# Performance work log

Hardware: AMD Instinct MI355X
Metric: run time of the kernel (lower is better)

Reference implementation:

```python
import jax, jax.numpy as jnp
import numpy as np

# ---- CRF hyperparameters (init_kwargs) ----
NUM_CLASSES = 4
RADIUS = 10            # guided filter radius -> 21x21 kernel
EPS = 1e-4
THETA_GAMMA = 2.5
G_RADIUS = int(THETA_GAMMA * 4)  # gaussian layer radius = 10 -> 21x21 kernel
SPATIAL_COMPAT = 3.0
BILATERAL_COMPAT = 10.0
NUM_ITERATIONS = 5
RGB_W = np.array([0.2989, 0.5870, 0.1140], dtype=np.float32)  # tf rgb_to_grayscale


def _make_kernel(radius, theta):
    x, y = np.mgrid[-radius:radius + 1, -radius:radius + 1]
    k = np.exp(-(x ** 2 + y ** 2) / (2.0 * theta ** 2))
    k = k / k.sum()
    k[radius, radius] = 0.0  # zero out center (no self-message)
    return jnp.asarray(k, dtype=jnp.float32)

_GAUSS_K = _make_kernel(G_RADIUS, THETA_GAMMA)          # spatial gaussian kernel
_GUIDED_K = _make_kernel(RADIUS, RADIUS / 3.0)          # guided-filter gaussian kernel


def _depthwise(src, k2d, r):
    # src: [B,H,W,C], k2d: [kh,kw]; zero-padded depthwise conv (same as pad+VALID)
    c = src.shape[-1]
    kh, kw = k2d.shape
    k = jnp.broadcast_to(k2d[:, :, None, None], (kh, kw, 1, c))
    return jax.lax.conv_general_dilated(
        src, k, window_strides=(1, 1), padding=[(r, r), (r, r)],
        dimension_numbers=('NHWC', 'HWIO', 'NHWC'), feature_group_count=c)


def _gaussian(src):
    return _depthwise(src, _GAUSS_K, G_RADIUS)


def _guided(gray, p):
    # guided gaussian filter with single-channel guide `gray` [B,H,W,1]
    gf = lambda s: _depthwise(s, _GUIDED_K, RADIUS)
    mean_I = gf(gray)                       # [B,H,W,1]
    mean_p = gf(p)                          # [B,H,W,C]
    mean_Ip = gf(gray * p)
    cov_Ip = mean_Ip - mean_I * mean_p
    mean_II = gf(gray * gray)
    var_I = mean_II - mean_I * mean_I
    a = cov_Ip / (var_I + EPS)
    b = mean_p - a * mean_I
    return gf(a) * gray + gf(b)


def setup_inputs() -> dict:
    key = jax.random.key(0)
    k1, k2 = jax.random.split(key)
    unary = jax.random.normal(k1, (1, 512, 512, NUM_CLASSES), dtype=jnp.float32)
    image = jax.random.uniform(k2, (1, 512, 512, 3), dtype=jnp.float32)
    return {"unary": unary, "image": image}


def reference(unary, image):
    gray = (image @ jnp.asarray(RGB_W))[..., None]        # [B,H,W,1]
    ones = jnp.ones_like(unary)
    spatial_norm = _gaussian(ones)
    bilateral_norm = _guided(gray, ones)

    Q = jax.nn.softmax(-unary, axis=-1)
    for _ in range(NUM_ITERATIONS):
        spatial_out = _gaussian(Q) / spatial_norm
        bilateral_out = _guided(gray, Q) / bilateral_norm
        # spatial_weights = SPATIAL_COMPAT*I, bilateral_weights = BILATERAL_COMPAT*I,
        # compatibility = -I  => matmuls reduce to scalar scaling + negation
        message = SPATIAL_COMPAT * spatial_out + BILATERAL_COMPAT * bilateral_out
        pairwise = -message
        Q = jax.nn.softmax(-unary - pairwise, axis=-1)
    return Q
```

## Files before the change

kernel.cpp:

```cpp
#include <hip/hip_runtime.h>
#include <math.h>

#define W 512
#define H 512
#define NPIX (W*H)
#define RAD 10
#define KS 21
#define CRF_EPS 1e-4f

#define TX 32
#define TY 16
#define CIN (TX + 2*RAD)
#define RIN (TY + 2*RAD)
#define GX (W / TX)
#define GY (H / TY)
#define NBLK (GX*GY)

struct W21 { float w[KS]; };

__device__ __forceinline__ float4 f4(float x, float y, float z, float w_) {
    return make_float4(x, y, z, w_);
}
__device__ __forceinline__ float4 fma4(float s, float4 a, float4 acc) {
    acc.x = fmaf(s, a.x, acc.x); acc.y = fmaf(s, a.y, acc.y);
    acc.z = fmaf(s, a.z, acc.z); acc.w = fmaf(s, a.w, acc.w);
    return acc;
}
__device__ __forceinline__ int swz(int b, int N) {
    return (b & 7) * (N >> 3) + (b >> 3);
}


__global__ __launch_bounds__(512) void k_tables(W21 wg, W21 wu, float* Sg, float* Su) {
    int x = threadIdx.x;
    float sg = 0.f, su = 0.f;
    #pragma unroll
    for (int d = -RAD; d <= RAD; ++d) {
        int xx = x + d;
        if (xx >= 0 && xx < W) { sg += wg.w[d + RAD]; su += wu.w[d + RAD]; }
    }
    Sg[x] = sg; Su[x] = su;
}

__global__ __launch_bounds__(256) void k_init(const float* __restrict__ img,
        const float4* __restrict__ unary, float* __restrict__ gray,
        float4* __restrict__ Q) {
    int b = swz(blockIdx.x, NPIX / 256);
    int p = b * 256 + threadIdx.x;
    float r = img[3 * p], g = img[3 * p + 1], bch = img[3 * p + 2];
    gray[p] = 0.2989f * r + 0.5870f * g + 0.1140f * bch;
    float4 u = unary[p];
    float mn = fminf(fminf(u.x, u.y), fminf(u.z, u.w));
    float ex = expf(mn - u.x), ey = expf(mn - u.y), ez = expf(mn - u.z), ew = expf(mn - u.w);
    float inv = 1.f / (ex + ey + ez + ew);
    Q[p] = f4(ex * inv, ey * inv, ez * inv, ew * inv);
}

__global__ __launch_bounds__(256) void k_s1(const float* __restrict__ gray,
        const float* __restrict__ Su, float* __restrict__ mean_I,
        float* __restrict__ inv_var, float2* __restrict__ a1b1,
        W21 wu, float c0u) {
    __shared__ float  sg[RIN][CIN];
    __shared__ float2 ii[TY][CIN];
    int L = swz(blockIdx.x, NBLK);
    int x0 = (L & (GX - 1)) * TX, y0 = (L >> 4) * TY;
    int t = threadIdx.x;
    for (int i = t; i < RIN * CIN; i += 256) {
        int r = i / CIN, c = i - r * CIN;
        int gx = x0 + c - RAD, gy = y0 + r - RAD;
        float g = 0.f;
        if ((unsigned)gx < W && (unsigned)gy < H) g = gray[gy * W + gx];
        sg[r][c] = g;
    }
    __syncthreads();
    for (int i = t; i < TY * CIN; i += 256) {
        int r = i / CIN, c = i - r * CIN;
        float vI = 0.f, vII = 0.f;
        #pragma unroll
        for (int d = 0; d < KS; ++d) {
            float g = sg[r + d][c];
            vI = fmaf(wu.w[d], g, vI);
            vII = fmaf(wu.w[d] * g, g, vII);
        }
        ii[r][c] = make_float2(vI, vII);
    }
    __syncthreads();
    int k = t & 15, ty = t >> 4, cb = 2 * k;
    float2 a0 = make_float2(0.f, 0.f), a1 = a0;
    #pragma unroll
    for (int d = 0; d < KS + 1; ++d) {
        float2 v = ii[ty][cb + d];
        if (d < KS) { a0.x = fmaf(wu.w[d], v.x, a0.x); a0.y = fmaf(wu.w[d], v.y, a0.y); }
        if (d > 0)  { a1.x = fmaf(wu.w[d-1], v.x, a1.x); a1.y = fmaf(wu.w[d-1], v.y, a1.y); }
    }
    int py = y0 + ty;
    float Suy = Su[py];
    #pragma unroll
    for (int j = 0; j < 2; ++j) {
        float2 acc = j ? a1 : a0;
        int px = x0 + cb + j;
        int p = py * W + px;
        float gc = sg[ty + RAD][cb + j + RAD];
        float mI = acc.x - c0u * gc;
        float mII = acc.y - c0u * gc * gc;
        float iv = 1.f / ((mII - mI * mI) + CRF_EPS);
        float N = Su[px] * Suy - c0u;
        float av = mI * (1.f - N) * iv;
        float bv = N - av * mI;
        mean_I[p] = mI; inv_var[p] = iv; a1b1[p] = make_float2(av, bv);
    }
}

__global__ __launch_bounds__(256) void k_s2(const float2* __restrict__ a1b1,
        const float* __restrict__ gray, float* __restrict__ inv_bn,
        W21 wu, float c0u) {
    __shared__ float2 s2[RIN][CIN];
    __shared__ float2 ii[TY][CIN];
    int L = swz(blockIdx.x, NBLK);
    int x0 = (L & (GX - 1)) * TX, y0 = (L >> 4) * TY;
    int t = threadIdx.x;
    for (int i = t; i < RIN * CIN; i += 256) {
        int r = i / CIN, c = i - r * CIN;
        int gx = x0 + c - RAD, gy = y0 + r - RAD;
        float2 v = make_float2(0.f, 0.f);
        if ((unsigned)gx < W && (unsigned)gy < H) v = a1b1[gy * W + gx];
        s2[r][c] = v;
    }
    __syncthreads();
    for (int i = t; i < TY * CIN; i += 256) {
        int r = i / CIN, c = i - r * CIN;
        float va = 0.f, vb = 0.f;
        #pragma unroll
        for (int d = 0; d < KS; ++d) {
            float2 v = s2[r + d][c];
            va = fmaf(wu.w[d], v.x, va);
            vb = fmaf(wu.w[d], v.y, vb);
        }
        ii[r][c] = make_float2(va, vb);
    }
    __syncthreads();
    int k = t & 15, ty = t >> 4, cb = 2 * k;
    float2 a0 = make_float2(0.f, 0.f), a1 = a0;
    #pragma unroll
    for (int d = 0; d < KS + 1; ++d) {
        float2 v = ii[ty][cb + d];
        if (d < KS) { a0.x = fmaf(wu.w[d], v.x, a0.x); a0.y = fmaf(wu.w[d], v.y, a0.y); }
        if (d > 0)  { a1.x = fmaf(wu.w[d-1], v.x, a1.x); a1.y = fmaf(wu.w[d-1], v.y, a1.y); }
    }
    int py = y0 + ty;
    #pragma unroll
    for (int j = 0; j < 2; ++j) {
        float2 acc = j ? a1 : a0;
        int px = x0 + cb + j;
        int p = py * W + px;
        float2 cen = s2[ty + RAD][cb + j + RAD];
        float va = acc.x - c0u * cen.x;
        float vb = acc.y - c0u * cen.y;
        inv_bn[p] = 1.f / (va * gray[p] + vb);
    }
}


__global__ __launch_bounds__(256) void k_f1(const float4* __restrict__ Q,
        const float* __restrict__ gray, const float* __restrict__ mean_I,
        const float* __restrict__ inv_var, const float* __restrict__ Sg,
        const float4* __restrict__ unary, float4* __restrict__ a_out,
        float4* __restrict__ b_out, float4* __restrict__ partial,
        W21 wg, W21 wu, float c0g, float c0u) {
    __shared__ float4 sQ[RIN][CIN];
    __shared__ float  sG[RIN][CIN];
    __shared__ float4 i0[TY][CIN];
    __shared__ float4 i1[TY][CIN];
    __shared__ float4 i2[TY][CIN];
    int L = swz(blockIdx.x, NBLK);
    int x0 = (L & (GX - 1)) * TX, y0 = (L >> 4) * TY;
    int t = threadIdx.x;
    for (int i = t; i < RIN * CIN; i += 256) {
        int r = i / CIN, c = i - r * CIN;
        int gx = x0 + c - RAD, gy = y0 + r - RAD;
        float4 q = f4(0.f, 0.f, 0.f, 0.f); float g = 0.f;
        if ((unsigned)gx < W && (unsigned)gy < H) {
            int p = gy * W + gx; q = Q[p]; g = gray[p];
        }
        sQ[r][c] = q; sG[r][c] = g;
    }
    __syncthreads();
    for (int i = t; i < TY * CIN; i += 256) {
        int r = i / CIN, c = i - r * CIN;
        float4 a0 = f4(0,0,0,0), a1 = a0, a2 = a0;
        #pragma unroll
        for (int d = 0; d < KS; ++d) {
            float4 q = sQ[r + d][c]; float g = sG[r + d][c];
            a0 = fma4(wg.w[d], q, a0);
            a1 = fma4(wu.w[d], q, a1);
            a2 = fma4(wu.w[d] * g, q, a2);
        }
        i0[r][c] = a0; i1[r][c] = a1; i2[r][c] = a2;
    }
    __syncthreads();
    int k = t & 15, ty = t >> 4, cb = 2 * k;
    float4 A0[2], A1[2], A2[2];
    #pragma unroll
    for (int j = 0; j < 2; ++j) { A0[j] = f4(0,0,0,0); A1[j] = A0[j]; A2[j] = A0[j]; }
    #pragma unroll
    for (int d = 0; d < KS + 1; ++d) {
        float4 v0 = i0[ty][cb + d], v1 = i1[ty][cb + d], v2 = i2[ty][cb + d];
        if (d < KS) {
            A0[0] = fma4(wg.w[d], v0, A0[0]);
            A1[0] = fma4(wu.w[d], v1, A1[0]);
            A2[0] = fma4(wu.w[d], v2, A2[0]);
        }
        if (d > 0) {
            A0[1] = fma4(wg.w[d-1], v0, A0[1]);
            A1[1] = fma4(wu.w[d-1], v1, A1[1]);
            A2[1] = fma4(wu.w[d-1], v2, A2[1]);
        }
    }
    int py = y0 + ty;
    float Sgy = Sg[py];
    #pragma unroll
    for (int j = 0; j < 2; ++j) {
        int px = x0 + cb + j;
        int p = py * W + px;
        float4 Qc = sQ[ty + RAD][cb + j + RAD];
        float gc = sG[ty + RAD][cb + j + RAD];
        float4 g4  = fma4(-c0g, Qc, A0[j]);
        float4 m4  = fma4(-c0u, Qc, A1[j]);
        float4 mi4 = fma4(-c0u * gc, Qc, A2[j]);
        float mI = mean_I[p], iv = inv_var[p];
        float4 a, b;
        a.x = (mi4.x - mI * m4.x) * iv; a.y = (mi4.y - mI * m4.y) * iv;
        a.z = (mi4.z - mI * m4.z) * iv; a.w = (mi4.w - mI * m4.w) * iv;
        b.x = m4.x - a.x * mI; b.y = m4.y - a.y * mI;
        b.z = m4.z - a.z * mI; b.w = m4.w - a.w * mI;
        float s3 = 3.f / (Sg[px] * Sgy - c0g);
        float4 u = unary[p];
        float4 part = f4(fmaf(s3, g4.x, -u.x), fmaf(s3, g4.y, -u.y),
                         fmaf(s3, g4.z, -u.z), fmaf(s3, g4.w, -u.w));
        a_out[p] = a; b_out[p] = b; partial[p] = part;
    }
}

__global__ __launch_bounds__(256) void k_f2(const float4* __restrict__ A,
        const float4* __restrict__ B, const float4* __restrict__ partial,
        const float* __restrict__ gray, const float* __restrict__ inv_bn,
        float4* __restrict__ Qout, W21 wu, float c0u) {
    __shared__ float4 sT[RIN][CIN];
    __shared__ float4 ia[TY][CIN];
    __shared__ float4 ib[TY][CIN];
    int L = swz(blockIdx.x, NBLK);
    int x0 = (L & (GX - 1)) * TX, y0 = (L >> 4) * TY;
    int t = threadIdx.x;
    int k = t & 15, ty = t >> 4, cb = 2 * k;
    for (int i = t; i < RIN * CIN; i += 256) {
        int r = i / CIN, c = i - r * CIN;
        int gx = x0 + c - RAD, gy = y0 + r - RAD;
        float4 v = f4(0.f, 0.f, 0.f, 0.f);
        if ((unsigned)gx < W && (unsigned)gy < H) v = A[gy * W + gx];
        sT[r][c] = v;
    }
    __syncthreads();
    float4 Ac[2];
    Ac[0] = sT[ty + RAD][cb + RAD]; Ac[1] = sT[ty + RAD][cb + 1 + RAD];
    for (int i = t; i < TY * CIN; i += 256) {
        int r = i / CIN, c = i - r * CIN;
        float4 acc = f4(0,0,0,0);
        #pragma unroll
        for (int d = 0; d < KS; ++d) acc = fma4(wu.w[d], sT[r + d][c], acc);
        ia[r][c] = acc;
    }
    __syncthreads();
    for (int i = t; i < RIN * CIN; i += 256) {
        int r = i / CIN, c = i - r * CIN;
        int gx = x0 + c - RAD, gy = y0 + r - RAD;
        float4 v = f4(0.f, 0.f, 0.f, 0.f);
        if ((unsigned)gx < W && (unsigned)gy < H) v = B[gy * W + gx];
        sT[r][c] = v;
    }
    __syncthreads();
    float4 Bc[2];
    Bc[0] = sT[ty + RAD][cb + RAD]; Bc[1] = sT[ty + RAD][cb + 1 + RAD];
    for (int i = t; i < TY * CIN; i += 256) {
        int r = i / CIN, c = i - r * CIN;
        float4 acc = f4(0,0,0,0);
        #pragma unroll
        for (int d = 0; d < KS; ++d) acc = fma4(wu.w[d], sT[r + d][c], acc);
        ib[r][c] = acc;
    }
    __syncthreads();
    float4 VA[2], VB[2];
    #pragma unroll
    for (int j = 0; j < 2; ++j) { VA[j] = f4(0,0,0,0); VB[j] = VA[j]; }
    #pragma unroll
    for (int d = 0; d < KS + 1; ++d) {
        float4 va = ia[ty][cb + d], vb = ib[ty][cb + d];
        if (d < KS) { VA[0] = fma4(wu.w[d], va, VA[0]); VB[0] = fma4(wu.w[d], vb, VB[0]); }
        if (d > 0)  { VA[1] = fma4(wu.w[d-1], va, VA[1]); VB[1] = fma4(wu.w[d-1], vb, VB[1]); }
    }
    int py = y0 + ty;
    #pragma unroll
    for (int j = 0; j < 2; ++j) {
        int px = x0 + cb + j;
        int p = py * W + px;
        float4 a4 = fma4(-c0u, Ac[j], VA[j]);
        float4 b4 = fma4(-c0u, Bc[j], VB[j]);
        float gv = gray[p];
        float ibn = 10.f * inv_bn[p];
        float4 part = partial[p];
        float lx = fmaf(fmaf(a4.x, gv, b4.x), ibn, part.x);
        float ly = fmaf(fmaf(a4.y, gv, b4.y), ibn, part.y);
        float lz = fmaf(fmaf(a4.z, gv, b4.z), ibn, part.z);
        float lw = fmaf(fmaf(a4.w, gv, b4.w), ibn, part.w);
        float m = fmaxf(fmaxf(lx, ly), fmaxf(lz, lw));
        float ex = expf(lx - m), ey = expf(ly - m), ez = expf(lz - m), ew = expf(lw - m);
        float inv = 1.f / (ex + ey + ez + ew);
        Qout[p] = f4(ex * inv, ey * inv, ez * inv, ew * inv);
    }
}


static void make_w_host(double theta, W21* w, float* c0) {
    double tmp[KS], s = 0.0;
    for (int d = -RAD; d <= RAD; ++d) {
        double v = exp(-(double)(d * d) / (2.0 * theta * theta));
        tmp[d + RAD] = v; s += v;
    }
    for (int i = 0; i < KS; ++i) w->w[i] = (float)(tmp[i] / s);
    *c0 = (float)(1.0 / (s * s));
}

extern "C" void kernel_launch(void* const* d_in, const int* in_sizes, int n_in,
                              void* d_out, int out_size, void* d_ws, size_t ws_size,
                              hipStream_t stream) {
    const float4* unary = (const float4*)d_in[0];
    const float* image = (const float*)d_in[1];
    float* wsf = (float*)d_ws;

    float*  gray    = wsf;
    float*  mean_I  = wsf + 262144;
    float*  inv_var = wsf + 524288;
    float2* a1b1    = (float2*)(wsf + 786432);
    float*  inv_bn  = wsf + 1310720;
    float*  Sg      = wsf + 1572864;
    float*  Su      = wsf + 1573376;
    float4* Q       = (float4*)(wsf + 1573888);
    float4* partial = (float4*)(wsf + 2622464);
    float4* a_arr   = (float4*)(wsf + 3671040);
    float4* b_arr   = (float4*)(wsf + 4719616);

    W21 wg, wu; float c0g, c0u;
    make_w_host(2.5, &wg, &c0g);
    make_w_host(10.0 / 3.0, &wu, &c0u);

    dim3 bl(256), grEl(NPIX / 256), grT(NBLK);

    k_tables<<<dim3(1), dim3(512), 0, stream>>>(wg, wu, Sg, Su);
    k_init<<<grEl, bl, 0, stream>>>(image, unary, gray, Q);
    k_s1<<<grT, bl, 0, stream>>>(gray, Su, mean_I, inv_var, a1b1, wu, c0u);
    k_s2<<<grT, bl, 0, stream>>>(a1b1, gray, inv_bn, wu, c0u);

    for (int it = 0; it < 5; ++it) {
        k_f1<<<grT, bl, 0, stream>>>((const float4*)Q, gray, mean_I, inv_var, Sg,
                                     unary, a_arr, b_arr, partial, wg, wu, c0g, c0u);
        float4* qdst = (it == 4) ? (float4*)d_out : Q;
        k_f2<<<grT, bl, 0, stream>>>(a_arr, b_arr, partial, gray, inv_bn, qdst,
                                     wu, c0u);
    }
}
```

Measured before the change: 197.7 us.

## Register-block separable convolution passes to reuse shared-memory loads across outputs

The vertical pass now has each thread compute 4 consecutive output rows for a column, sliding over 24 shared-memory rows in registers. The horizontal pass has each thread compute 4 adjacent outputs from 24 loads. This applies to all stencil kernels. It cuts shared-memory reads per output by reusing each load for up to four outputs. In exchange, fewer threads are active (208 and 128 of 256), so latency hiding drops, and register pressure rises, most in k_f1 with 12 float4 accumulators.

```diff
diff --git a/kernel.cpp b/kernel.cpp
--- a/kernel.cpp
+++ b/kernel.cpp
@@ -15,6 +15,7 @@
 #define GX (W / TX)
 #define GY (H / TY)
 #define NBLK (GX*GY)
+#define NVT (CIN * 4)
 
 struct W21 { float w[KS]; };
 
@@ -73,41 +74,60 @@
         sg[r][c] = g;
     }
     __syncthreads();
-    for (int i = t; i < TY * CIN; i += 256) {
-        int r = i / CIN, c = i - r * CIN;
-        float vI = 0.f, vII = 0.f;
-        #pragma unroll
-        for (int d = 0; d < KS; ++d) {
-            float g = sg[r + d][c];
-            vI = fmaf(wu.w[d], g, vI);
-            vII = fmaf(wu.w[d] * g, g, vII);
-        }
-        ii[r][c] = make_float2(vI, vII);
-    }
-    __syncthreads();
-    int k = t & 15, ty = t >> 4, cb = 2 * k;
-    float2 a0 = make_float2(0.f, 0.f), a1 = a0;
-    #pragma unroll
-    for (int d = 0; d < KS + 1; ++d) {
-        float2 v = ii[ty][cb + d];
-        if (d < KS) { a0.x = fmaf(wu.w[d], v.x, a0.x); a0.y = fmaf(wu.w[d], v.y, a0.y); }
-        if (d > 0)  { a1.x = fmaf(wu.w[d-1], v.x, a1.x); a1.y = fmaf(wu.w[d-1], v.y, a1.y); }
-    }
-    int py = y0 + ty;
-    float Suy = Su[py];
-    #pragma unroll
-    for (int j = 0; j < 2; ++j) {
-        float2 acc = j ? a1 : a0;
-        int px = x0 + cb + j;
-        int p = py * W + px;
-        float gc = sg[ty + RAD][cb + j + RAD];
-        float mI = acc.x - c0u * gc;
-        float mII = acc.y - c0u * gc * gc;
-        float iv = 1.f / ((mII - mI * mI) + CRF_EPS);
-        float N = Su[px] * Suy - c0u;
-        float av = mI * (1.f - N) * iv;
-        float bv = N - av * mI;
-        mean_I[p] = mI; inv_var[p] = iv; a1b1[p] = make_float2(av, bv);
+    if (t < NVT) {
+        int c = t % CIN, rg = t / CIN, r0 = rg * 4;
+        float2 acc[4];
+        #pragma unroll
+        for (int j = 0; j < 4; ++j) acc[j] = make_float2(0.f, 0.f);
+        #pragma unroll
+        for (int s = 0; s < 24; ++s) {
+            float g = sg[r0 + s][c];
+            #pragma unroll
+            for (int j = 0; j < 4; ++j) {
+                int d = s - j;
+                if (d >= 0 && d <= 20) {
+                    float wg_ = wu.w[d] * g;
+                    acc[j].x += wg_;
+                    acc[j].y = fmaf(wg_, g, acc[j].y);
+                }
+            }
+        }
+        #pragma unroll
+        for (int j = 0; j < 4; ++j) ii[r0 + j][c] = acc[j];
+    }
+    __syncthreads();
+    if (t < 128) {
+        int row = t >> 3, c0 = (t & 7) * 4;
+        float2 A[4];
+        #pragma unroll
+        for (int j = 0; j < 4; ++j) A[j] = make_float2(0.f, 0.f);
+        #pragma unroll
+        for (int s = 0; s < 24; ++s) {
+            float2 v = ii[row][c0 + s];
+            #pragma unroll
+            for (int j = 0; j < 4; ++j) {
+                int d = s - j;
+                if (d >= 0 && d <= 20) {
+                    A[j].x = fmaf(wu.w[d], v.x, A[j].x);
+                    A[j].y = fmaf(wu.w[d], v.y, A[j].y);
+                }
+            }
+        }
+        int py = y0 + row;
+        float Suy = Su[py];
+        #pragma unroll
+        for (int j = 0; j < 4; ++j) {
+            int px = x0 + c0 + j;
+            int p = py * W + px;
+            float gc = sg[row + RAD][c0 + j + RAD];
+            float mI = A[j].x - c0u * gc;
+            float mII = A[j].y - c0u * gc * gc;
+            float iv = 1.f / ((mII - mI * mI) + CRF_EPS);
+            float N = Su[px] * Suy - c0u;
+            float av = mI * (1.f - N) * iv;
+            float bv = N - av * mI;
+            mean_I[p] = mI; inv_var[p] = iv; a1b1[p] = make_float2(av, bv);
+        }
     }
 }
 
@@ -127,36 +147,54 @@
         s2[r][c] = v;
     }
     __syncthreads();
-    for (int i = t; i < TY * CIN; i += 256) {
-        int r = i / CIN, c = i - r * CIN;
-        float va = 0.f, vb = 0.f;
-        #pragma unroll
-        for (int d = 0; d < KS; ++d) {
-            float2 v = s2[r + d][c];
-            va = fmaf(wu.w[d], v.x, va);
-            vb = fmaf(wu.w[d], v.y, vb);
-        }
-        ii[r][c] = make_float2(va, vb);
-    }
-    __syncthreads();
-    int k = t & 15, ty = t >> 4, cb = 2 * k;
-    float2 a0 = make_float2(0.f, 0.f), a1 = a0;
-    #pragma unroll
-    for (int d = 0; d < KS + 1; ++d) {
-        float2 v = ii[ty][cb + d];
-        if (d < KS) { a0.x = fmaf(wu.w[d], v.x, a0.x); a0.y = fmaf(wu.w[d], v.y, a0.y); }
-        if (d > 0)  { a1.x = fmaf(wu.w[d-1], v.x, a1.x); a1.y = fmaf(wu.w[d-1], v.y, a1.y); }
-    }
-    int py = y0 + ty;
-    #pragma unroll
-    for (int j = 0; j < 2; ++j) {
-        float2 acc = j ? a1 : a0;
-        int px = x0 + cb + j;
-        int p = py * W + px;
-        float2 cen = s2[ty + RAD][cb + j + RAD];
-        float va = acc.x - c0u * cen.x;
-        float vb = acc.y - c0u * cen.y;
-        inv_bn[p] = 1.f / (va * gray[p] + vb);
+    if (t < NVT) {
+        int c = t % CIN, rg = t / CIN, r0 = rg * 4;
+        float2 acc[4];
+        #pragma unroll
+        for (int j = 0; j < 4; ++j) acc[j] = make_float2(0.f, 0.f);
+        #pragma unroll
+        for (int s = 0; s < 24; ++s) {
+            float2 v = s2[r0 + s][c];
+            #pragma unroll
+            for (int j = 0; j < 4; ++j) {
+                int d = s - j;
+                if (d >= 0 && d <= 20) {
+                    acc[j].x = fmaf(wu.w[d], v.x, acc[j].x);
+                    acc[j].y = fmaf(wu.w[d], v.y, acc[j].y);
+                }
+            }
+        }
+        #pragma unroll
+        for (int j = 0; j < 4; ++j) ii[r0 + j][c] = acc[j];
+    }
+    __syncthreads();
+    if (t < 128) {
+        int row = t >> 3, c0 = (t & 7) * 4;
+        float2 A[4];
+        #pragma unroll
+        for (int j = 0; j < 4; ++j) A[j] = make_float2(0.f, 0.f);
+        #pragma unroll
+        for (int s = 0; s < 24; ++s) {
+            float2 v = ii[row][c0 + s];
+            #pragma unroll
+            for (int j = 0; j < 4; ++j) {
+                int d = s - j;
+                if (d >= 0 && d <= 20) {
+                    A[j].x = fmaf(wu.w[d], v.x, A[j].x);
+                    A[j].y = fmaf(wu.w[d], v.y, A[j].y);
+                }
+            }
+        }
+        int py = y0 + row;
+        #pragma unroll
+        for (int j = 0; j < 4; ++j) {
+            int px = x0 + c0 + j;
+            int p = py * W + px;
+            float2 cen = s2[row + RAD][c0 + j + RAD];
+            float va = A[j].x - c0u * cen.x;
+            float vb = A[j].y - c0u * cen.y;
+            inv_bn[p] = 1.f / (va * gray[p] + vb);
+        }
     }
 }
 
@@ -185,59 +223,72 @@
         sQ[r][c] = q; sG[r][c] = g;
     }
     __syncthreads();
-    for (int i = t; i < TY * CIN; i += 256) {
-        int r = i / CIN, c = i - r * CIN;
-        float4 a0 = f4(0,0,0,0), a1 = a0, a2 = a0;
-        #pragma unroll
-        for (int d = 0; d < KS; ++d) {
-            float4 q = sQ[r + d][c]; float g = sG[r + d][c];
-            a0 = fma4(wg.w[d], q, a0);
-            a1 = fma4(wu.w[d], q, a1);
-            a2 = fma4(wu.w[d] * g, q, a2);
-        }
-        i0[r][c] = a0; i1[r][c] = a1; i2[r][c] = a2;
-    }
-    __syncthreads();
-    int k = t & 15, ty = t >> 4, cb = 2 * k;
-    float4 A0[2], A1[2], A2[2];
-    #pragma unroll
-    for (int j = 0; j < 2; ++j) { A0[j] = f4(0,0,0,0); A1[j] = A0[j]; A2[j] = A0[j]; }
-    #pragma unroll
-    for (int d = 0; d < KS + 1; ++d) {
-        float4 v0 = i0[ty][cb + d], v1 = i1[ty][cb + d], v2 = i2[ty][cb + d];
-        if (d < KS) {
-            A0[0] = fma4(wg.w[d], v0, A0[0]);
-            A1[0] = fma4(wu.w[d], v1, A1[0]);
-            A2[0] = fma4(wu.w[d], v2, A2[0]);
-        }
-        if (d > 0) {
-            A0[1] = fma4(wg.w[d-1], v0, A0[1]);
-            A1[1] = fma4(wu.w[d-1], v1, A1[1]);
-            A2[1] = fma4(wu.w[d-1], v2, A2[1]);
-        }
-    }
-    int py = y0 + ty;
-    float Sgy = Sg[py];
-    #pragma unroll
-    for (int j = 0; j < 2; ++j) {
-        int px = x0 + cb + j;
-        int p = py * W + px;
-        float4 Qc = sQ[ty + RAD][cb + j + RAD];
-        float gc = sG[ty + RAD][cb + j + RAD];
-        float4 g4  = fma4(-c0g, Qc, A0[j]);
-        float4 m4  = fma4(-c0u, Qc, A1[j]);
-        float4 mi4 = fma4(-c0u * gc, Qc, A2[j]);
-        float mI = mean_I[p], iv = inv_var[p];
-        float4 a, b;
-        a.x = (mi4.x - mI * m4.x) * iv; a.y = (mi4.y - mI * m4.y) * iv;
-        a.z = (mi4.z - mI * m4.z) * iv; a.w = (mi4.w - mI * m4.w) * iv;
-        b.x = m4.x - a.x * mI; b.y = m4.y - a.y * mI;
-        b.z = m4.z - a.z * mI; b.w = m4.w - a.w * mI;
-        float s3 = 3.f / (Sg[px] * Sgy - c0g);
-        float4 u = unary[p];
-        float4 part = f4(fmaf(s3, g4.x, -u.x), fmaf(s3, g4.y, -u.y),
-                         fmaf(s3, g4.z, -u.z), fmaf(s3, g4.w, -u.w));
-        a_out[p] = a; b_out[p] = b; partial[p] = part;
+    if (t < NVT) {
+        int c = t % CIN, rg = t / CIN, r0 = rg * 4;
+        float4 a0[4], a1[4], a2[4];
+        #pragma unroll
+        for (int j = 0; j < 4; ++j) { a0[j] = f4(0,0,0,0); a1[j] = a0[j]; a2[j] = a0[j]; }
+        #pragma unroll
+        for (int s = 0; s < 24; ++s) {
+            float4 q = sQ[r0 + s][c]; float g = sG[r0 + s][c];
+            float4 gq = f4(g * q.x, g * q.y, g * q.z, g * q.w);
+            #pragma unroll
+            for (int j = 0; j < 4; ++j) {
+                int d = s - j;
+                if (d >= 0 && d <= 20) {
+                    a0[j] = fma4(wg.w[d], q, a0[j]);
+                    a1[j] = fma4(wu.w[d], q, a1[j]);
+                    a2[j] = fma4(wu.w[d], gq, a2[j]);
+                }
+            }
+        }
+        #pragma unroll
+        for (int j = 0; j < 4; ++j) {
+            i0[r0 + j][c] = a0[j]; i1[r0 + j][c] = a1[j]; i2[r0 + j][c] = a2[j];
+        }
+    }
+    __syncthreads();
+    if (t < 128) {
+        int row = t >> 3, c0 = (t & 7) * 4;
+        float4 A0[4], A1[4], A2[4];
+        #pragma unroll
+        for (int j = 0; j < 4; ++j) { A0[j] = f4(0,0,0,0); A1[j] = A0[j]; A2[j] = A0[j]; }
+        #pragma unroll
+        for (int s = 0; s < 24; ++s) {
+            float4 v0 = i0[row][c0 + s], v1 = i1[row][c0 + s], v2 = i2[row][c0 + s];
+            #pragma unroll
+            for (int j = 0; j < 4; ++j) {
+                int d = s - j;
+                if (d >= 0 && d <= 20) {
+                    A0[j] = fma4(wg.w[d], v0, A0[j]);
+                    A1[j] = fma4(wu.w[d], v1, A1[j]);
+                    A2[j] = fma4(wu.w[d], v2, A2[j]);
+                }
+            }
+        }
+        int py = y0 + row;
+        float Sgy = Sg[py];
+        #pragma unroll
+        for (int j = 0; j < 4; ++j) {
+            int px = x0 + c0 + j;
+            int p = py * W + px;
+            float4 Qc = sQ[row + RAD][c0 + j + RAD];
+            float gc = sG[row + RAD][c0 + j + RAD];
+            float4 g4  = fma4(-c0g, Qc, A0[j]);
+            float4 m4  = fma4(-c0u, Qc, A1[j]);
+            float4 mi4 = fma4(-c0u * gc, Qc, A2[j]);
+            float mI = mean_I[p], iv = inv_var[p];
+            float4 a, b;
+            a.x = (mi4.x - mI * m4.x) * iv; a.y = (mi4.y - mI * m4.y) * iv;
+            a.z = (mi4.z - mI * m4.z) * iv; a.w = (mi4.w - mI * m4.w) * iv;
+            b.x = m4.x - a.x * mI; b.y = m4.y - a.y * mI;
+            b.z = m4.z - a.z * mI; b.w = m4.w - a.w * mI;
+            float s3 = 3.f / (Sg[px] * Sgy - c0g);
+            float4 u = unary[p];
+            float4 part = f4(fmaf(s3, g4.x, -u.x), fmaf(s3, g4.y, -u.y),
+                             fmaf(s3, g4.z, -u.z), fmaf(s3, g4.w, -u.w));
+            a_out[p] = a; b_out[p] = b; partial[p] = part;
+        }
     }
 }
 
@@ -251,7 +302,8 @@
     int L = swz(blockIdx.x, NBLK);
     int x0 = (L & (GX - 1)) * TX, y0 = (L >> 4) * TY;
     int t = threadIdx.x;
-    int k = t & 15, ty = t >> 4, cb = 2 * k;
+    int vc = t % CIN, vrg = t / CIN, vr0 = vrg * 4;
+    int row = t >> 3, c0 = (t & 7) * 4;
     for (int i = t; i < RIN * CIN; i += 256) {
         int r = i / CIN, c = i - r * CIN;
         int gx = x0 + c - RAD, gy = y0 + r - RAD;
@@ -260,14 +312,26 @@
         sT[r][c] = v;
     }
     __syncthreads();
-    float4 Ac[2];
-    Ac[0] = sT[ty + RAD][cb + RAD]; Ac[1] = sT[ty + RAD][cb + 1 + RAD];
-    for (int i = t; i < TY * CIN; i += 256) {
-        int r = i / CIN, c = i - r * CIN;
-        float4 acc = f4(0,0,0,0);
-        #pragma unroll
-        for (int d = 0; d < KS; ++d) acc = fma4(wu.w[d], sT[r + d][c], acc);
-        ia[r][c] = acc;
+    float4 Ac[4];
+    if (t < 128) {
+        #pragma unroll
+        for (int j = 0; j < 4; ++j) Ac[j] = sT[row + RAD][c0 + j + RAD];
+    }
+    if (t < NVT) {
+        float4 acc[4];
+        #pragma unroll
+        for (int j = 0; j < 4; ++j) acc[j] = f4(0,0,0,0);
+        #pragma unroll
+        for (int s = 0; s < 24; ++s) {
+            float4 v = sT[vr0 + s][vc];
+            #pragma unroll
+            for (int j = 0; j < 4; ++j) {
+                int d = s - j;
+                if (d >= 0 && d <= 20) acc[j] = fma4(wu.w[d], v, acc[j]);
+            }
+        }
+        #pragma unroll
+        for (int j = 0; j < 4; ++j) ia[vr0 + j][vc] = acc[j];
     }
     __syncthreads();
     for (int i = t; i < RIN * CIN; i += 256) {
@@ -278,43 +342,59 @@
         sT[r][c] = v;
     }
     __syncthreads();
-    float4 Bc[2];
-    Bc[0] = sT[ty + RAD][cb + RAD]; Bc[1] = sT[ty + RAD][cb + 1 + RAD];
-    for (int i = t; i < TY * CIN; i += 256) {
-        int r = i / CIN, c = i - r * CIN;
-        float4 acc = f4(0,0,0,0);
-        #pragma unroll
-        for (int d = 0; d < KS; ++d) acc = fma4(wu.w[d], sT[r + d][c], acc);
-        ib[r][c] = acc;
-    }
-    __syncthreads();
-    float4 VA[2], VB[2];
-    #pragma unroll
-    for (int j = 0; j < 2; ++j) { VA[j] = f4(0,0,0,0); VB[j] = VA[j]; }
-    #pragma unroll
-    for (int d = 0; d < KS + 1; ++d) {
-        float4 va = ia[ty][cb + d], vb = ib[ty][cb + d];
-        if (d < KS) { VA[0] = fma4(wu.w[d], va, VA[0]); VB[0] = fma4(wu.w[d], vb, VB[0]); }
-        if (d > 0)  { VA[1] = fma4(wu.w[d-1], va, VA[1]); VB[1] = fma4(wu.w[d-1], vb, VB[1]); }
-    }
-    int py = y0 + ty;
-    #pragma unroll
-    for (int j = 0; j < 2; ++j) {
-        int px = x0 + cb + j;
-        int p = py * W + px;
-        float4 a4 = fma4(-c0u, Ac[j], VA[j]);
-        float4 b4 = fma4(-c0u, Bc[j], VB[j]);
-        float gv = gray[p];
-        float ibn = 10.f * inv_bn[p];
-        float4 part = partial[p];
-        float lx = fmaf(fmaf(a4.x, gv, b4.x), ibn, part.x);
-        float ly = fmaf(fmaf(a4.y, gv, b4.y), ibn, part.y);
-        float lz = fmaf(fmaf(a4.z, gv, b4.z), ibn, part.z);
-        float lw = fmaf(fmaf(a4.w, gv, b4.w), ibn, part.w);
-        float m = fmaxf(fmaxf(lx, ly), fmaxf(lz, lw));
-        float ex = expf(lx - m), ey = expf(ly - m), ez = expf(lz - m), ew = expf(lw - m);
-        float inv = 1.f / (ex + ey + ez + ew);
-        Qout[p] = f4(ex * inv, ey * inv, ez * inv, ew * inv);
+    if (t < NVT) {
+        float4 acc[4];
+        #pragma unroll
+        for (int j = 0; j < 4; ++j) acc[j] = f4(0,0,0,0);
+        #pragma unroll
+        for (int s = 0; s < 24; ++s) {
+            float4 v = sT[vr0 + s][vc];
+            #pragma unroll
+            for (int j = 0; j < 4; ++j) {
+                int d = s - j;
+                if (d >= 0 && d <= 20) acc[j] = fma4(wu.w[d], v, acc[j]);
+            }
+        }
+        #pragma unroll
+        for (int j = 0; j < 4; ++j) ib[vr0 + j][vc] = acc[j];
+    }
+    __syncthreads();
+    if (t < 128) {
+        float4 VA[4], VB[4];
+        #pragma unroll
+        for (int j = 0; j < 4; ++j) { VA[j] = f4(0,0,0,0); VB[j] = VA[j]; }
+        #pragma unroll
+        for (int s = 0; s < 24; ++s) {
+            float4 va = ia[row][c0 + s], vb = ib[row][c0 + s];
+            #pragma unroll
+            for (int j = 0; j < 4; ++j) {
+                int d = s - j;
+                if (d >= 0 && d <= 20) {
+                    VA[j] = fma4(wu.w[d], va, VA[j]);
+                    VB[j] = fma4(wu.w[d], vb, VB[j]);
+                }
+            }
+        }
+        int py = y0 + row;
+        #pragma unroll
+        for (int j = 0; j < 4; ++j) {
+            int px = x0 + c0 + j;
+            int p = py * W + px;
+            float4 Bc = sT[row + RAD][c0 + j + RAD];
+            float4 a4 = fma4(-c0u, Ac[j], VA[j]);
+            float4 b4 = fma4(-c0u, Bc, VB[j]);
+            float gv = gray[p];
+            float ibn = 10.f * inv_bn[p];
+            float4 part = partial[p];
+            float lx = fmaf(fmaf(a4.x, gv, b4.x), ibn, part.x);
+            float ly = fmaf(fmaf(a4.y, gv, b4.y), ibn, part.y);
+            float lz = fmaf(fmaf(a4.z, gv, b4.z), ibn, part.z);
+            float lw = fmaf(fmaf(a4.w, gv, b4.w), ibn, part.w);
+            float m = fmaxf(fmaxf(lx, ly), fmaxf(lz, lw));
+            float ex = expf(lx - m), ey = expf(ly - m), ez = expf(lz - m), ew = expf(lw - m);
+            float inv = 1.f / (ex + ey + ez + ew);
+            Qout[p] = f4(ex * inv, ey * inv, ez * inv, ew * inv);
+        }
     }
 }
 
```

Measured after the change: 202.6 us. 2.5% more time.

## Halve tile height, alias shared buffers, and fold table setup into init

Applied to the files above, without the earlier changes.

Tile height drops from 16 to 8 rows. That doubles the block count and, together with aliasing intermediate shared buffers over the input tile, cuts per-block LDS so that `__launch_bounds__(256,4)` can target four blocks per CU. The vertical pass now has 208 threads each compute two adjacent output rows from a 22-row sliding window. The horizontal pass gives one pixel per thread instead of two. The separate k_tables launch is folded into k_init. The trade-off is a larger halo overhead per tile (28 loaded rows for 8 output rows) and idle threads during the vertical pass, in exchange for better occupancy and latency hiding.

```diff
diff --git a/kernel.cpp b/kernel.cpp
--- a/kernel.cpp
+++ b/kernel.cpp
@@ -9,12 +9,13 @@
 #define CRF_EPS 1e-4f
 
 #define TX 32
-#define TY 16
+#define TY 8
 #define CIN (TX + 2*RAD)
 #define RIN (TY + 2*RAD)
 #define GX (W / TX)
 #define GY (H / TY)
 #define NBLK (GX*GY)
+#define NVT (CIN * 4)
 
 struct W21 { float w[KS]; };
 
@@ -31,22 +32,23 @@
 }
 
 
-__global__ __launch_bounds__(512) void k_tables(W21 wg, W21 wu, float* Sg, float* Su) {
-    int x = threadIdx.x;
-    float sg = 0.f, su = 0.f;
-    #pragma unroll
-    for (int d = -RAD; d <= RAD; ++d) {
-        int xx = x + d;
-        if (xx >= 0 && xx < W) { sg += wg.w[d + RAD]; su += wu.w[d + RAD]; }
-    }
-    Sg[x] = sg; Su[x] = su;
-}
-
 __global__ __launch_bounds__(256) void k_init(const float* __restrict__ img,
         const float4* __restrict__ unary, float* __restrict__ gray,
-        float4* __restrict__ Q) {
+        float4* __restrict__ Q, float* __restrict__ Sg, float* __restrict__ Su,
+        W21 wg, W21 wu) {
+    int t = threadIdx.x;
+    if (blockIdx.x < 2) {
+        int x = blockIdx.x * 256 + t;
+        float sg = 0.f, su = 0.f;
+        #pragma unroll
+        for (int d = -RAD; d <= RAD; ++d) {
+            int xx = x + d;
+            if (xx >= 0 && xx < W) { sg += wg.w[d + RAD]; su += wu.w[d + RAD]; }
+        }
+        Sg[x] = sg; Su[x] = su;
+    }
     int b = swz(blockIdx.x, NPIX / 256);
-    int p = b * 256 + threadIdx.x;
+    int p = b * 256 + t;
     float r = img[3 * p], g = img[3 * p + 1], bch = img[3 * p + 2];
     gray[p] = 0.2989f * r + 0.5870f * g + 0.1140f * bch;
     float4 u = unary[p];
@@ -56,7 +58,7 @@
     Q[p] = f4(ex * inv, ey * inv, ez * inv, ew * inv);
 }
 
-__global__ __launch_bounds__(256) void k_s1(const float* __restrict__ gray,
+__global__ __launch_bounds__(256, 4) void k_s1(const float* __restrict__ gray,
         const float* __restrict__ Su, float* __restrict__ mean_I,
         float* __restrict__ inv_var, float2* __restrict__ a1b1,
         W21 wu, float c0u) {
@@ -73,45 +75,40 @@
         sg[r][c] = g;
     }
     __syncthreads();
-    for (int i = t; i < TY * CIN; i += 256) {
-        int r = i / CIN, c = i - r * CIN;
-        float vI = 0.f, vII = 0.f;
-        #pragma unroll
-        for (int d = 0; d < KS; ++d) {
-            float g = sg[r + d][c];
-            vI = fmaf(wu.w[d], g, vI);
-            vII = fmaf(wu.w[d] * g, g, vII);
-        }
-        ii[r][c] = make_float2(vI, vII);
-    }
-    __syncthreads();
-    int k = t & 15, ty = t >> 4, cb = 2 * k;
-    float2 a0 = make_float2(0.f, 0.f), a1 = a0;
+    if (t < NVT) {
+        int c = t % CIN, r0 = (t / CIN) * 2;
+        float2 acc[2];
+        acc[0] = make_float2(0.f, 0.f); acc[1] = acc[0];
+        #pragma unroll
+        for (int s = 0; s < 22; ++s) {
+            float g = sg[r0 + s][c];
+            if (s <= 20) { float wg_ = wu.w[s] * g; acc[0].x += wg_; acc[0].y = fmaf(wg_, g, acc[0].y); }
+            if (s >= 1)  { float wg_ = wu.w[s-1] * g; acc[1].x += wg_; acc[1].y = fmaf(wg_, g, acc[1].y); }
+        }
+        ii[r0][c] = acc[0]; ii[r0 + 1][c] = acc[1];
+    }
+    __syncthreads();
+    int row = t >> 5, col = t & 31;
+    float2 A = make_float2(0.f, 0.f);
     #pragma unroll
-    for (int d = 0; d < KS + 1; ++d) {
-        float2 v = ii[ty][cb + d];
-        if (d < KS) { a0.x = fmaf(wu.w[d], v.x, a0.x); a0.y = fmaf(wu.w[d], v.y, a0.y); }
-        if (d > 0)  { a1.x = fmaf(wu.w[d-1], v.x, a1.x); a1.y = fmaf(wu.w[d-1], v.y, a1.y); }
-    }
-    int py = y0 + ty;
-    float Suy = Su[py];
-    #pragma unroll
-    for (int j = 0; j < 2; ++j) {
-        float2 acc = j ? a1 : a0;
-        int px = x0 + cb + j;
-        int p = py * W + px;
-        float gc = sg[ty + RAD][cb + j + RAD];
-        float mI = acc.x - c0u * gc;
-        float mII = acc.y - c0u * gc * gc;
-        float iv = 1.f / ((mII - mI * mI) + CRF_EPS);
-        float N = Su[px] * Suy - c0u;
-        float av = mI * (1.f - N) * iv;
-        float bv = N - av * mI;
-        mean_I[p] = mI; inv_var[p] = iv; a1b1[p] = make_float2(av, bv);
-    }
-}
-
-__global__ __launch_bounds__(256) void k_s2(const float2* __restrict__ a1b1,
+    for (int d = 0; d < KS; ++d) {
+        float2 v = ii[row][col + d];
+        A.x = fmaf(wu.w[d], v.x, A.x);
+        A.y = fmaf(wu.w[d], v.y, A.y);
+    }
+    int py = y0 + row, px = x0 + col;
+    int p = py * W + px;
+    float gc = sg[row + RAD][col + RAD];
+    float mI = A.x - c0u * gc;
+    float mII = A.y - c0u * gc * gc;
+    float iv = 1.f / ((mII - mI * mI) + CRF_EPS);
+    float N = Su[px] * Su[py] - c0u;
+    float av = mI * (1.f - N) * iv;
+    float bv = N - av * mI;
+    mean_I[p] = mI; inv_var[p] = iv; a1b1[p] = make_float2(av, bv);
+}
+
+__global__ __launch_bounds__(256, 4) void k_s2(const float2* __restrict__ a1b1,
         const float* __restrict__ gray, float* __restrict__ inv_bn,
         W21 wu, float c0u) {
     __shared__ float2 s2[RIN][CIN];
@@ -127,51 +124,47 @@
         s2[r][c] = v;
     }
     __syncthreads();
-    for (int i = t; i < TY * CIN; i += 256) {
-        int r = i / CIN, c = i - r * CIN;
-        float va = 0.f, vb = 0.f;
-        #pragma unroll
-        for (int d = 0; d < KS; ++d) {
-            float2 v = s2[r + d][c];
-            va = fmaf(wu.w[d], v.x, va);
-            vb = fmaf(wu.w[d], v.y, vb);
-        }
-        ii[r][c] = make_float2(va, vb);
-    }
-    __syncthreads();
-    int k = t & 15, ty = t >> 4, cb = 2 * k;
-    float2 a0 = make_float2(0.f, 0.f), a1 = a0;
+    if (t < NVT) {
+        int c = t % CIN, r0 = (t / CIN) * 2;
+        float2 acc[2];
+        acc[0] = make_float2(0.f, 0.f); acc[1] = acc[0];
+        #pragma unroll
+        for (int s = 0; s < 22; ++s) {
+            float2 v = s2[r0 + s][c];
+            if (s <= 20) { acc[0].x = fmaf(wu.w[s], v.x, acc[0].x); acc[0].y = fmaf(wu.w[s], v.y, acc[0].y); }
+            if (s >= 1)  { acc[1].x = fmaf(wu.w[s-1], v.x, acc[1].x); acc[1].y = fmaf(wu.w[s-1], v.y, acc[1].y); }
+        }
+        ii[r0][c] = acc[0]; ii[r0 + 1][c] = acc[1];
+    }
+    __syncthreads();
+    int row = t >> 5, col = t & 31;
+    float2 A = make_float2(0.f, 0.f);
     #pragma unroll
-    for (int d = 0; d < KS + 1; ++d) {
-        float2 v = ii[ty][cb + d];
-        if (d < KS) { a0.x = fmaf(wu.w[d], v.x, a0.x); a0.y = fmaf(wu.w[d], v.y, a0.y); }
-        if (d > 0)  { a1.x = fmaf(wu.w[d-1], v.x, a1.x); a1.y = fmaf(wu.w[d-1], v.y, a1.y); }
-    }
-    int py = y0 + ty;
-    #pragma unroll
-    for (int j = 0; j < 2; ++j) {
-        float2 acc = j ? a1 : a0;
-        int px = x0 + cb + j;
-        int p = py * W + px;
-        float2 cen = s2[ty + RAD][cb + j + RAD];
-        float va = acc.x - c0u * cen.x;
-        float vb = acc.y - c0u * cen.y;
-        inv_bn[p] = 1.f / (va * gray[p] + vb);
-    }
-}
-
-
-__global__ __launch_bounds__(256) void k_f1(const float4* __restrict__ Q,
+    for (int d = 0; d < KS; ++d) {
+        float2 v = ii[row][col + d];
+        A.x = fmaf(wu.w[d], v.x, A.x);
+        A.y = fmaf(wu.w[d], v.y, A.y);
+    }
+    int p = (y0 + row) * W + x0 + col;
+    float2 cen = s2[row + RAD][col + RAD];
+    float va = A.x - c0u * cen.x;
+    float vb = A.y - c0u * cen.y;
+    inv_bn[p] = 1.f / (va * gray[p] + vb);
+}
+
+
+__global__ __launch_bounds__(256, 4) void k_f1(const float4* __restrict__ Q,
         const float* __restrict__ gray, const float* __restrict__ mean_I,
         const float* __restrict__ inv_var, const float* __restrict__ Sg,
         const float4* __restrict__ unary, float4* __restrict__ a_out,
         float4* __restrict__ b_out, float4* __restrict__ partial,
         W21 wg, W21 wu, float c0g, float c0u) {
-    __shared__ float4 sQ[RIN][CIN];
-    __shared__ float  sG[RIN][CIN];
-    __shared__ float4 i0[TY][CIN];
-    __shared__ float4 i1[TY][CIN];
-    __shared__ float4 i2[TY][CIN];
+    __shared__ __align__(16) char smem[23296 + 5824 + 6656];
+    float4* sQ = (float4*)smem;
+    float*  sG = (float*)(smem + 23296);
+    float4* i2 = (float4*)(smem + 23296 + 5824);
+    float4* i0 = (float4*)smem;
+    float4* i1 = (float4*)(smem + 6656);
     int L = swz(blockIdx.x, NBLK);
     int x0 = (L & (GX - 1)) * TX, y0 = (L >> 4) * TY;
     int t = threadIdx.x;
@@ -182,92 +175,108 @@
         if ((unsigned)gx < W && (unsigned)gy < H) {
             int p = gy * W + gx; q = Q[p]; g = gray[p];
         }
-        sQ[r][c] = q; sG[r][c] = g;
-    }
-    __syncthreads();
-    for (int i = t; i < TY * CIN; i += 256) {
-        int r = i / CIN, c = i - r * CIN;
-        float4 a0 = f4(0,0,0,0), a1 = a0, a2 = a0;
-        #pragma unroll
-        for (int d = 0; d < KS; ++d) {
-            float4 q = sQ[r + d][c]; float g = sG[r + d][c];
-            a0 = fma4(wg.w[d], q, a0);
-            a1 = fma4(wu.w[d], q, a1);
-            a2 = fma4(wu.w[d] * g, q, a2);
-        }
-        i0[r][c] = a0; i1[r][c] = a1; i2[r][c] = a2;
-    }
-    __syncthreads();
-    int k = t & 15, ty = t >> 4, cb = 2 * k;
-    float4 A0[2], A1[2], A2[2];
+        sQ[i] = q; sG[i] = g;
+    }
+    __syncthreads();
+    int row = t >> 5, col = t & 31;
+    int py = y0 + row, px = x0 + col;
+    int p = py * W + px;
+    float mI = mean_I[p], iv = inv_var[p];
+    float4 u = unary[p];
+    float sgx = Sg[px], sgy = Sg[py];
+    float4 Qc = sQ[(row + RAD) * CIN + col + RAD];
+    float  gc = sG[(row + RAD) * CIN + col + RAD];
+    float4 a0[2], a1[2], a2[2];
+    int vc = t % CIN, vr0 = (t / CIN) * 2;
+    if (t < NVT) {
+        #pragma unroll
+        for (int j = 0; j < 2; ++j) { a0[j] = f4(0,0,0,0); a1[j] = a0[j]; a2[j] = a0[j]; }
+        #pragma unroll
+        for (int s = 0; s < 22; ++s) {
+            float4 q = sQ[(vr0 + s) * CIN + vc];
+            float g = sG[(vr0 + s) * CIN + vc];
+            float4 gq = f4(g * q.x, g * q.y, g * q.z, g * q.w);
+            if (s <= 20) {
+                a0[0] = fma4(wg.w[s], q, a0[0]);
+                a1[0] = fma4(wu.w[s], q, a1[0]);
+                a2[0] = fma4(wu.w[s], gq, a2[0]);
+            }
+            if (s >= 1) {
+                a0[1] = fma4(wg.w[s-1], q, a0[1]);
+                a1[1] = fma4(wu.w[s-1], q, a1[1]);
+                a2[1] = fma4(wu.w[s-1], gq, a2[1]);
+            }
+        }
+    }
+    __syncthreads();
+    if (t < NVT) {
+        #pragma unroll
+        for (int j = 0; j < 2; ++j) {
+            i0[(vr0 + j) * CIN + vc] = a0[j];
+            i1[(vr0 + j) * CIN + vc] = a1[j];
+            i2[(vr0 + j) * CIN + vc] = a2[j];
+        }
+    }
+    __syncthreads();
+    float4 A0 = f4(0,0,0,0), A1 = A0, A2 = A0;
     #pragma unroll
-    for (int j = 0; j < 2; ++j) { A0[j] = f4(0,0,0,0); A1[j] = A0[j]; A2[j] = A0[j]; }
-    #pragma unroll
-    for (int d = 0; d < KS + 1; ++d) {
-        float4 v0 = i0[ty][cb + d], v1 = i1[ty][cb + d], v2 = i2[ty][cb + d];
-        if (d < KS) {
-            A0[0] = fma4(wg.w[d], v0, A0[0]);
-            A1[0] = fma4(wu.w[d], v1, A1[0]);
-            A2[0] = fma4(wu.w[d], v2, A2[0]);
-        }
-        if (d > 0) {
-            A0[1] = fma4(wg.w[d-1], v0, A0[1]);
-            A1[1] = fma4(wu.w[d-1], v1, A1[1]);
-            A2[1] = fma4(wu.w[d-1], v2, A2[1]);
-        }
-    }
-    int py = y0 + ty;
-    float Sgy = Sg[py];
-    #pragma unroll
-    for (int j = 0; j < 2; ++j) {
-        int px = x0 + cb + j;
-        int p = py * W + px;
-        float4 Qc = sQ[ty + RAD][cb + j + RAD];
-        float gc = sG[ty + RAD][cb + j + RAD];
-        float4 g4  = fma4(-c0g, Qc, A0[j]);
-        float4 m4  = fma4(-c0u, Qc, A1[j]);
-        float4 mi4 = fma4(-c0u * gc, Qc, A2[j]);
-        float mI = mean_I[p], iv = inv_var[p];
-        float4 a, b;
-        a.x = (mi4.x - mI * m4.x) * iv; a.y = (mi4.y - mI * m4.y) * iv;
-        a.z = (mi4.z - mI * m4.z) * iv; a.w = (mi4.w - mI * m4.w) * iv;
-        b.x = m4.x - a.x * mI; b.y = m4.y - a.y * mI;
-        b.z = m4.z - a.z * mI; b.w = m4.w - a.w * mI;
-        float s3 = 3.f / (Sg[px] * Sgy - c0g);
-        float4 u = unary[p];
-        float4 part = f4(fmaf(s3, g4.x, -u.x), fmaf(s3, g4.y, -u.y),
-                         fmaf(s3, g4.z, -u.z), fmaf(s3, g4.w, -u.w));
-        a_out[p] = a; b_out[p] = b; partial[p] = part;
-    }
-}
-
-__global__ __launch_bounds__(256) void k_f2(const float4* __restrict__ A,
+    for (int d = 0; d < KS; ++d) {
+        A0 = fma4(wg.w[d], i0[row * CIN + col + d], A0);
+        A1 = fma4(wu.w[d], i1[row * CIN + col + d], A1);
+        A2 = fma4(wu.w[d], i2[row * CIN + col + d], A2);
+    }
+    float4 g4  = fma4(-c0g, Qc, A0);
+    float4 m4  = fma4(-c0u, Qc, A1);
+    float4 mi4 = fma4(-c0u * gc, Qc, A2);
+    float4 a, b;
+    a.x = (mi4.x - mI * m4.x) * iv; a.y = (mi4.y - mI * m4.y) * iv;
+    a.z = (mi4.z - mI * m4.z) * iv; a.w = (mi4.w - mI * m4.w) * iv;
+    b.x = m4.x - a.x * mI; b.y = m4.y - a.y * mI;
+    b.z = m4.z - a.z * mI; b.w = m4.w - a.w * mI;
+    float s3 = 3.f / (sgx * sgy - c0g);
+    float4 part = f4(fmaf(s3, g4.x, -u.x), fmaf(s3, g4.y, -u.y),
+                     fmaf(s3, g4.z, -u.z), fmaf(s3, g4.w, -u.w));
+    a_out[p] = a; b_out[p] = b; partial[p] = part;
+}
+
+__global__ __launch_bounds__(256, 4) void k_f2(const float4* __restrict__ A,
         const float4* __restrict__ B, const float4* __restrict__ partial,
         const float* __restrict__ gray, const float* __restrict__ inv_bn,
         float4* __restrict__ Qout, W21 wu, float c0u) {
-    __shared__ float4 sT[RIN][CIN];
-    __shared__ float4 ia[TY][CIN];
-    __shared__ float4 ib[TY][CIN];
+    __shared__ __align__(16) char smem[23296 + 6656];
+    float4* sT = (float4*)smem;
+    float4* ia = (float4*)(smem + 23296);
+    float4* ib = (float4*)smem;
     int L = swz(blockIdx.x, NBLK);
     int x0 = (L & (GX - 1)) * TX, y0 = (L >> 4) * TY;
     int t = threadIdx.x;
-    int k = t & 15, ty = t >> 4, cb = 2 * k;
+    int row = t >> 5, col = t & 31;
+    int py = y0 + row, px = x0 + col;
+    int p = py * W + px;
+    int vc = t % CIN, vr0 = (t / CIN) * 2;
+    float gv = gray[p];
+    float ibn = 10.f * inv_bn[p];
+    float4 part = partial[p];
     for (int i = t; i < RIN * CIN; i += 256) {
         int r = i / CIN, c = i - r * CIN;
         int gx = x0 + c - RAD, gy = y0 + r - RAD;
         float4 v = f4(0.f, 0.f, 0.f, 0.f);
         if ((unsigned)gx < W && (unsigned)gy < H) v = A[gy * W + gx];
-        sT[r][c] = v;
-    }
-    __syncthreads();
-    float4 Ac[2];
-    Ac[0] = sT[ty + RAD][cb + RAD]; Ac[1] = sT[ty + RAD][cb + 1 + RAD];
-    for (int i = t; i < TY * CIN; i += 256) {
-        int r = i / CIN, c = i - r * CIN;
-        float4 acc = f4(0,0,0,0);
-        #pragma unroll
-        for (int d = 0; d < KS; ++d) acc = fma4(wu.w[d], sT[r + d][c], acc);
-        ia[r][c] = acc;
+        sT[i] = v;
+    }
+    __syncthreads();
+    float4 Ac = sT[(row + RAD) * CIN + col + RAD];
+    float4 va[2];
+    va[0] = f4(0,0,0,0); va[1] = va[0];
+    if (t < NVT) {
+        #pragma unroll
+        for (int s = 0; s < 22; ++s) {
+            float4 v = sT[(vr0 + s) * CIN + vc];
+            if (s <= 20) va[0] = fma4(wu.w[s], v, va[0]);
+            if (s >= 1)  va[1] = fma4(wu.w[s-1], v, va[1]);
+        }
+        ia[vr0 * CIN + vc] = va[0];
+        ia[(vr0 + 1) * CIN + vc] = va[1];
     }
     __syncthreads();
     for (int i = t; i < RIN * CIN; i += 256) {
@@ -275,47 +284,42 @@
         int gx = x0 + c - RAD, gy = y0 + r - RAD;
         float4 v = f4(0.f, 0.f, 0.f, 0.f);
         if ((unsigned)gx < W && (unsigned)gy < H) v = B[gy * W + gx];
-        sT[r][c] = v;
-    }
-    __syncthreads();
-    float4 Bc[2];
-    Bc[0] = sT[ty + RAD][cb + RAD]; Bc[1] = sT[ty + RAD][cb + 1 + RAD];
-    for (int i = t; i < TY * CIN; i += 256) {
-        int r = i / CIN, c = i - r * CIN;
-        float4 acc = f4(0,0,0,0);
-        #pragma unroll
-        for (int d = 0; d < KS; ++d) acc = fma4(wu.w[d], sT[r + d][c], acc);
-        ib[r][c] = acc;
-    }
-    __syncthreads();
-    float4 VA[2], VB[2];
+        sT[i] = v;
+    }
+    __syncthreads();
+    float4 Bc = sT[(row + RAD) * CIN + col + RAD];
+    float4 vb[2];
+    vb[0] = f4(0,0,0,0); vb[1] = vb[0];
+    if (t < NVT) {
+        #pragma unroll
+        for (int s = 0; s < 22; ++s) {
+            float4 v = sT[(vr0 + s) * CIN + vc];
+            if (s <= 20) vb[0] = fma4(wu.w[s], v, vb[0]);
+            if (s >= 1)  vb[1] = fma4(wu.w[s-1], v, vb[1]);
+        }
+    }
+    __syncthreads();
+    if (t < NVT) {
+        ib[vr0 * CIN + vc] = vb[0];
+        ib[(vr0 + 1) * CIN + vc] = vb[1];
+    }
+    __syncthreads();
+    float4 VA = f4(0,0,0,0), VB = VA;
     #pragma unroll
-    for (int j = 0; j < 2; ++j) { VA[j] = f4(0,0,0,0); VB[j] = VA[j]; }
-    #pragma unroll
-    for (int d = 0; d < KS + 1; ++d) {
-        float4 va = ia[ty][cb + d], vb = ib[ty][cb + d];
-        if (d < KS) { VA[0] = fma4(wu.w[d], va, VA[0]); VB[0] = fma4(wu.w[d], vb, VB[0]); }
-        if (d > 0)  { VA[1] = fma4(wu.w[d-1], va, VA[1]); VB[1] = fma4(wu.w[d-1], vb, VB[1]); }
-    }
-    int py = y0 + ty;
-    #pragma unroll
-    for (int j = 0; j < 2; ++j) {
-        int px = x0 + cb + j;
-        int p = py * W + px;
-        float4 a4 = fma4(-c0u, Ac[j], VA[j]);
-        float4 b4 = fma4(-c0u, Bc[j], VB[j]);
-        float gv = gray[p];
-        float ibn = 10.f * inv_bn[p];
-        float4 part = partial[p];
-        float lx = fmaf(fmaf(a4.x, gv, b4.x), ibn, part.x);
-        float ly = fmaf(fmaf(a4.y, gv, b4.y), ibn, part.y);
-        float lz = fmaf(fmaf(a4.z, gv, b4.z), ibn, part.z);
-        float lw = fmaf(fmaf(a4.w, gv, b4.w), ibn, part.w);
-        float m = fmaxf(fmaxf(lx, ly), fmaxf(lz, lw));
-        float ex = expf(lx - m), ey = expf(ly - m), ez = expf(lz - m), ew = expf(lw - m);
-        float inv = 1.f / (ex + ey + ez + ew);
-        Qout[p] = f4(ex * inv, ey * inv, ez * inv, ew * inv);
-    }
+    for (int d = 0; d < KS; ++d) {
+        VA = fma4(wu.w[d], ia[row * CIN + col + d], VA);
+        VB = fma4(wu.w[d], ib[row * CIN + col + d], VB);
+    }
+    float4 a4 = fma4(-c0u, Ac, VA);
+    float4 b4 = fma4(-c0u, Bc, VB);
+    float lx = fmaf(fmaf(a4.x, gv, b4.x), ibn, part.x);
+    float ly = fmaf(fmaf(a4.y, gv, b4.y), ibn, part.y);
+    float lz = fmaf(fmaf(a4.z, gv, b4.z), ibn, part.z);
+    float lw = fmaf(fmaf(a4.w, gv, b4.w), ibn, part.w);
+    float m = fmaxf(fmaxf(lx, ly), fmaxf(lz, lw));
+    float ex = expf(lx - m), ey = expf(ly - m), ez = expf(lz - m), ew = expf(lw - m);
+    float inv = 1.f / (ex + ey + ez + ew);
+    Qout[p] = f4(ex * inv, ey * inv, ez * inv, ew * inv);
 }
 
 
@@ -354,8 +358,7 @@
 
     dim3 bl(256), grEl(NPIX / 256), grT(NBLK);
 
-    k_tables<<<dim3(1), dim3(512), 0, stream>>>(wg, wu, Sg, Su);
-    k_init<<<grEl, bl, 0, stream>>>(image, unary, gray, Q);
+    k_init<<<grEl, bl, 0, stream>>>(image, unary, gray, Q, Sg, Su, wg, wu);
     k_s1<<<grT, bl, 0, stream>>>(gray, Su, mean_I, inv_var, a1b1, wu, c0u);
     k_s2<<<grT, bl, 0, stream>>>(a1b1, gray, inv_bn, wu, c0u);
 
```

Result: faster. 173.5 us (-12.3%).
